# Performance work log

Hardware: AMD Instinct MI355X
Metric: run time of the kernel (lower is better)

## Reference

```python
import jax, jax.numpy as jnp
import numpy as np

N = 10000      # nodes
E = 160000     # edges (before self loops)
F_IN = 78      # atom features
C = 128        # output_dim per head
H = 10         # heads in gat1
G = 64         # graphs in batch


def gat_conv(x, src, dst, n_nodes, W, a_src, a_dst, heads, ch):
    # x: [N, Fin]; W: [Fin, heads*ch]; a_src/a_dst: [heads, ch]
    h = (x @ W).reshape(-1, heads, ch)                      # [N, H, C]
    alpha_src = (h * a_src).sum(-1)                         # [N, H]
    alpha_dst = (h * a_dst).sum(-1)                         # [N, H]
    e = jax.nn.leaky_relu(alpha_src[src] + alpha_dst[dst], 0.2)  # [E, H]
    # segment softmax over edges grouped by destination node
    m = jax.ops.segment_max(e, dst, num_segments=n_nodes)
    m = jnp.where(jnp.isfinite(m), m, 0.0)
    ex = jnp.exp(e - m[dst])
    den = jax.ops.segment_sum(ex, dst, num_segments=n_nodes)
    alpha = ex / (den[dst] + 1e-16)                         # [E, H]
    out = jax.ops.segment_sum(h[src] * alpha[:, :, None], dst,
                              num_segments=n_nodes)          # [N, H, C]
    return out, alpha


def setup_inputs() -> dict:
    key = jax.random.key(0)
    ks = jax.random.split(key, 12)
    x = jax.random.normal(ks[0], (N, F_IN), dtype=jnp.float32)
    edge_index = jax.random.randint(ks[1], (2, E), 0, N, dtype=jnp.int64)
    batch = jnp.sort(jax.random.randint(ks[2], (N,), 0, G, dtype=jnp.int64))
    s1 = 1.0 / np.sqrt(F_IN)
    s2 = 1.0 / np.sqrt(H * C)
    W1 = jax.random.normal(ks[3], (F_IN, H * C), jnp.float32) * s1
    att_src1 = jax.random.normal(ks[4], (H, C), jnp.float32) * 0.1
    att_dst1 = jax.random.normal(ks[5], (H, C), jnp.float32) * 0.1
    b1 = jnp.zeros((H * C,), jnp.float32)
    W2 = jax.random.normal(ks[6], (H * C, C), jnp.float32) * s2
    att_src2 = jax.random.normal(ks[7], (1, C), jnp.float32) * 0.1
    att_dst2 = jax.random.normal(ks[8], (1, C), jnp.float32) * 0.1
    b2 = jnp.zeros((C,), jnp.float32)
    return {"x": x, "edge_index": edge_index, "batch": batch,
            "W1": W1, "att_src1": att_src1, "att_dst1": att_dst1, "b1": b1,
            "W2": W2, "att_src2": att_src2, "att_dst2": att_dst2, "b2": b2}


def reference(x, edge_index, batch, W1, att_src1, att_dst1, b1,
              W2, att_src2, att_dst2, b2):
    n = x.shape[0]
    loops = jnp.arange(n, dtype=edge_index.dtype)
    src = jnp.concatenate([edge_index[0], loops])  # PyG adds self loops
    dst = jnp.concatenate([edge_index[1], loops])
    # layer 1: 10 heads, concat
    h1, alpha1 = gat_conv(x, src, dst, n, W1, att_src1, att_dst1, H, C)
    h1 = jax.nn.elu(h1.reshape(n, H * C) + b1)     # dropout skipped (eval)
    # layer 2: 1 head
    h2, _ = gat_conv(h1, src, dst, n, W2, att_src2, att_dst2, 1, C)
    h2 = jax.nn.elu(h2.reshape(n, C) + b2)
    # global max pool per graph
    pooled = jax.ops.segment_max(h2, batch, num_segments=G)  # [G, C]
    return pooled, alpha1
```

## Files before the change

kernel.cpp:

```cpp
#include <hip/hip_runtime.h>
#include <hip/hip_bf16.h>

#define FIN 78
#define CDIM 128
#define HEADS 10
#define HC 1280
#define GRAPHS 64
#define KP 96

typedef __bf16 bf16x8 __attribute__((ext_vector_type(8)));
typedef __bf16 bf16x4 __attribute__((ext_vector_type(4)));
typedef float f32x4 __attribute__((ext_vector_type(4)));

__global__ void init_kernel(unsigned* counts, unsigned* cursor, unsigned* pooled_u,
                            float* h2p, float* as1, float* ad1, float* as2, float* ad2,
                            const float* __restrict__ x, __bf16* __restrict__ xb,
                            const float* __restrict__ W1, __bf16* __restrict__ W1t,
                            const float* __restrict__ W2, __bf16* __restrict__ W2t,
                            int N, int Mpad) {
    int t = blockIdx.x * 256 + threadIdx.x;
    if (t < N) { counts[t] = 0u; cursor[t] = 0u; as2[t] = 0.f; ad2[t] = 0.f; }
    if (t < GRAPHS * CDIM) pooled_u[t] = 0x007FFFFFu;
    if (t < N * CDIM) h2p[t] = 0.f;
    if (t < N * HEADS) { as1[t] = 0.f; ad1[t] = 0.f; }
    if (t < Mpad * KP) {
        int m = t / KP, k = t % KP;
        float v = (m < N && k < FIN) ? x[(size_t)m * FIN + k] : 0.f;
        xb[t] = (__bf16)v;
    }
    if (t < HC * KP) {
        int n = t / KP, k = t % KP;
        float v = (k < FIN) ? W1[(size_t)k * HC + n] : 0.f;
        W1t[t] = (__bf16)v;
    }
    if (t < CDIM * HC) {
        int n = t / HC, k = t % HC;
        W2t[t] = (__bf16)W2[(size_t)k * CDIM + n];
    }
}

__global__ __launch_bounds__(256) void gemm1_mfma_kernel(
        const __bf16* __restrict__ xb, const __bf16* __restrict__ W1t,
        const float* __restrict__ asrc, const float* __restrict__ adst,
        __bf16* __restrict__ h1pb, float* __restrict__ as1, float* __restrict__ ad1,
        int M) {
    __shared__ __align__(16) __bf16 Alds[128][104];
    __shared__ __align__(16) __bf16 Blds[128][104];
    const int tid = threadIdx.x;
    const int wave = tid >> 6, lane = tid & 63;
    const int wr = wave >> 1, wc = wave & 1;
    const int m0 = blockIdx.x * 128;
    const int head = blockIdx.y;
    const int n0 = head * CDIM;
    const int fl = lane & 15;
    const int fh = lane >> 4;

    for (int idx = tid; idx < 128 * 12; idx += 256) {
        int r = idx / 12, ks = (idx % 12) * 8;
        *(bf16x8*)&Alds[r][ks] = *(const bf16x8*)(xb + (size_t)(m0 + r) * KP + ks);
        *(bf16x8*)&Blds[r][ks] = *(const bf16x8*)(W1t + (size_t)(n0 + r) * KP + ks);
    }
    __syncthreads();

    f32x4 acc[4][4] = {};
    #pragma unroll
    for (int ks = 0; ks < KP; ks += 32) {
        bf16x8 a[4], b[4];
        #pragma unroll
        for (int t = 0; t < 4; ++t) {
            a[t] = *(const bf16x8*)&Alds[wr * 64 + t * 16 + fl][ks + fh * 8];
            b[t] = *(const bf16x8*)&Blds[wc * 64 + t * 16 + fl][ks + fh * 8];
        }
        #pragma unroll
        for (int i = 0; i < 4; ++i)
            #pragma unroll
            for (int j = 0; j < 4; ++j)
                acc[i][j] = __builtin_amdgcn_mfma_f32_16x16x32_bf16(a[i], b[j], acc[i][j], 0, 0, 0);
    }

    float a_s[4], a_d[4];
    #pragma unroll
    for (int j = 0; j < 4; ++j) {
        int gn = n0 + wc * 64 + j * 16 + fl;
        a_s[j] = asrc[gn];
        a_d[j] = adst[gn];
    }
    #pragma unroll
    for (int i = 0; i < 4; ++i) {
        #pragma unroll
        for (int r = 0; r < 4; ++r) {
            int gm = m0 + wr * 64 + i * 16 + fh * 4 + r;
            bool ok = gm < M;
            float vs = 0.f, vd = 0.f;
            #pragma unroll
            for (int j = 0; j < 4; ++j) {
                float v = acc[i][j][r];
                if (ok) h1pb[(size_t)gm * HC + n0 + wc * 64 + j * 16 + fl] = (__bf16)v;
                vs += v * a_s[j];
                vd += v * a_d[j];
            }
            #pragma unroll
            for (int off = 1; off < 16; off <<= 1) {
                vs += __shfl_xor(vs, off);
                vd += __shfl_xor(vd, off);
            }
            if (fl == 0 && ok) {
                atomicAdd(&as1[gm * HEADS + head], vs);
                atomicAdd(&ad1[gm * HEADS + head], vd);
            }
        }
    }
}

__global__ __launch_bounds__(256) void gemm2_mfma_kernel(
        const __bf16* __restrict__ A, const __bf16* __restrict__ W2t,
        const float* __restrict__ asrc2, const float* __restrict__ adst2,
        float* __restrict__ C, float* __restrict__ as2, float* __restrict__ ad2, int M) {
    constexpr int BK = 64;
    constexpr int KCHUNK = HC / 2;
    __shared__ __align__(16) __bf16 Alds[64][BK + 8];
    __shared__ __align__(16) __bf16 Blds[64][BK + 8];
    const int tid = threadIdx.x;
    const int wave = tid >> 6, lane = tid & 63;
    const int wr = wave >> 1, wc = wave & 1;
    const int m0 = blockIdx.x * 64;
    const int n0 = blockIdx.y * 64;
    const int kbase = blockIdx.z * KCHUNK;

    const int kslot = (tid & 7) * 8;
    const int srow  = tid >> 3;
    const int fl = lane & 15;
    const int fh = lane >> 4;

    f32x4 acc[2][2] = {};

    for (int k0 = kbase; k0 < kbase + KCHUNK; k0 += BK) {
        #pragma unroll
        for (int rp = 0; rp < 2; ++rp) {
            int r = srow + rp * 32;
            int gm = m0 + r;
            bf16x8 va = {};
            if (gm < M) va = *(const bf16x8*)(A + (size_t)gm * HC + k0 + kslot);
            *(bf16x8*)&Alds[r][kslot] = va;
            *(bf16x8*)&Blds[r][kslot] = *(const bf16x8*)(W2t + (size_t)(n0 + r) * HC + k0 + kslot);
        }
        __syncthreads();
        #pragma unroll
        for (int ks = 0; ks < BK; ks += 32) {
            bf16x8 a[2], b[2];
            #pragma unroll
            for (int t = 0; t < 2; ++t) {
                a[t] = *(const bf16x8*)&Alds[wr * 32 + t * 16 + fl][ks + fh * 8];
                b[t] = *(const bf16x8*)&Blds[wc * 32 + t * 16 + fl][ks + fh * 8];
            }
            #pragma unroll
            for (int i = 0; i < 2; ++i)
                #pragma unroll
                for (int j = 0; j < 2; ++j)
                    acc[i][j] = __builtin_amdgcn_mfma_f32_16x16x32_bf16(a[i], b[j], acc[i][j], 0, 0, 0);
        }
        __syncthreads();
    }
    const int gn0 = n0 + wc * 32 + fl;
    const int gn1 = gn0 + 16;
    const float a_s0 = asrc2[gn0], a_s1 = asrc2[gn1];
    const float a_d0 = adst2[gn0], a_d1 = adst2[gn1];
    #pragma unroll
    for (int i = 0; i < 2; ++i)
        #pragma unroll
        for (int r = 0; r < 4; ++r) {
            int gm = m0 + wr * 32 + i * 16 + fh * 4 + r;
            if (gm < M) {
                atomicAdd(&C[(size_t)gm * CDIM + gn0], acc[i][0][r]);
                atomicAdd(&C[(size_t)gm * CDIM + gn1], acc[i][1][r]);
            }
            float vs = acc[i][0][r] * a_s0 + acc[i][1][r] * a_s1;
            float vd = acc[i][0][r] * a_d0 + acc[i][1][r] * a_d1;
            #pragma unroll
            for (int off = 1; off < 16; off <<= 1) {
                vs += __shfl_xor(vs, off);
                vd += __shfl_xor(vd, off);
            }
            if (fl == 0 && gm < M) {
                atomicAdd(&as2[gm], vs);
                atomicAdd(&ad2[gm], vd);
            }
        }
}

__global__ void hist_kernel(const int* __restrict__ ei, int E, int N, unsigned* counts) {
    int e = blockIdx.x * 256 + threadIdx.x;
    int Et = E + N;
    if (e >= Et) return;
    int d = (e < E) ? ei[E + e] : (e - E);
    atomicAdd(&counts[d], 1u);
}

__global__ void scan_kernel(const unsigned* __restrict__ counts, unsigned* __restrict__ offsets, int n) {
    __shared__ unsigned part[1024];
    int t = threadIdx.x;
    int chunk = (n + 1023) / 1024;
    int lo = t * chunk, hi = min(lo + chunk, n);
    unsigned s = 0;
    for (int i = lo; i < hi; ++i) s += counts[i];
    part[t] = s;
    __syncthreads();
    for (int d = 1; d < 1024; d <<= 1) {
        unsigned v = (t >= d) ? part[t - d] : 0u;
        __syncthreads();
        part[t] += v;
        __syncthreads();
    }
    unsigned base = (t == 0) ? 0u : part[t - 1];
    for (int i = lo; i < hi; ++i) { offsets[i] = base; base += counts[i]; }
    if (t == 1023) offsets[n] = part[1023];
}

__global__ void scatter_kernel(const int* __restrict__ ei, int E, int N,
                               const unsigned* __restrict__ offsets, unsigned* cursor,
                               int* __restrict__ csr_src, int* __restrict__ csr_eid) {
    int e = blockIdx.x * 256 + threadIdx.x;
    int Et = E + N;
    if (e >= Et) return;
    int s, d;
    if (e < E) { s = ei[e]; d = ei[E + e]; } else { s = e - E; d = e - E; }
    unsigned pos = offsets[d] + atomicAdd(&cursor[d], 1u);
    csr_src[pos] = s;
    csr_eid[pos] = e;
}

__global__ __launch_bounds__(256) void softmax1_kernel(
        const unsigned* __restrict__ offsets,
        const int* __restrict__ csr_src, const int* __restrict__ csr_eid,
        const float* __restrict__ as1, const float* __restrict__ ad1,
        float* __restrict__ alpha_out, float* __restrict__ alpha_csr, int N) {
    const int wave = threadIdx.x >> 6, lane = threadIdx.x & 63;
    const int n = blockIdx.x * 4 + wave;
    if (n >= N) return;
    const unsigned p0 = offsets[n], p1 = offsets[n + 1];
    const unsigned deg = p1 - p0;

    float adn[HEADS];
    #pragma unroll
    for (int h = 0; h < HEADS; ++h) adn[h] = ad1[n * HEADS + h];

    if (deg <= 64) {
        const bool act = lane < (int)deg;
        const unsigned p = p0 + lane;
        int s = 0, eid = 0;
        if (act) { s = csr_src[p]; eid = csr_eid[p]; }
        const float* arow = as1 + (size_t)s * HEADS;
        float e[HEADS];
        #pragma unroll
        for (int h = 0; h < HEADS; ++h) {
            float v = act ? (arow[h] + adn[h]) : -INFINITY;
            e[h] = (v >= 0.f) ? v : 0.2f * v;
        }
        float m[HEADS];
        #pragma unroll
        for (int h = 0; h < HEADS; ++h) m[h] = e[h];
        #pragma unroll
        for (int off = 32; off; off >>= 1)
            #pragma unroll
            for (int h = 0; h < HEADS; ++h) m[h] = fmaxf(m[h], __shfl_xor(m[h], off));
        float ex[HEADS], sm[HEADS];
        #pragma unroll
        for (int h = 0; h < HEADS; ++h) {
            ex[h] = act ? __expf(e[h] - m[h]) : 0.f;
            sm[h] = ex[h];
        }
        #pragma unroll
        for (int off = 32; off; off >>= 1)
            #pragma unroll
            for (int h = 0; h < HEADS; ++h) sm[h] += __shfl_xor(sm[h], off);
        if (act) {
            #pragma unroll
            for (int h = 0; h < HEADS; ++h) {
                float a = ex[h] / (sm[h] + 1e-16f);
                alpha_csr[(size_t)p * HEADS + h] = a;
                alpha_out[(size_t)eid * HEADS + h] = a;
            }
        }
    } else {
        float m[HEADS];
        #pragma unroll
        for (int h = 0; h < HEADS; ++h) m[h] = -INFINITY;
        for (unsigned p = p0 + lane; p < p1; p += 64) {
            const float* arow = as1 + (size_t)csr_src[p] * HEADS;
            #pragma unroll
            for (int h = 0; h < HEADS; ++h) {
                float v = arow[h] + adn[h];
                v = (v >= 0.f) ? v : 0.2f * v;
                m[h] = fmaxf(m[h], v);
            }
        }
        #pragma unroll
        for (int off = 32; off; off >>= 1)
            #pragma unroll
            for (int h = 0; h < HEADS; ++h) m[h] = fmaxf(m[h], __shfl_xor(m[h], off));
        float sm[HEADS];
        #pragma unroll
        for (int h = 0; h < HEADS; ++h) sm[h] = 0.f;
        for (unsigned p = p0 + lane; p < p1; p += 64) {
            const float* arow = as1 + (size_t)csr_src[p] * HEADS;
            #pragma unroll
            for (int h = 0; h < HEADS; ++h) {
                float v = arow[h] + adn[h];
                v = (v >= 0.f) ? v : 0.2f * v;
                sm[h] += __expf(v - m[h]);
            }
        }
        #pragma unroll
        for (int off = 32; off; off >>= 1)
            #pragma unroll
            for (int h = 0; h < HEADS; ++h) sm[h] += __shfl_xor(sm[h], off);
        float inv[HEADS];
        #pragma unroll
        for (int h = 0; h < HEADS; ++h) inv[h] = 1.f / (sm[h] + 1e-16f);
        for (unsigned p = p0 + lane; p < p1; p += 64) {
            const float* arow = as1 + (size_t)csr_src[p] * HEADS;
            int eid = csr_eid[p];
            #pragma unroll
            for (int h = 0; h < HEADS; ++h) {
                float v = arow[h] + adn[h];
                v = (v >= 0.f) ? v : 0.2f * v;
                float a = __expf(v - m[h]) * inv[h];
                alpha_csr[(size_t)p * HEADS + h] = a;
                alpha_out[(size_t)eid * HEADS + h] = a;
            }
        }
    }
}

__global__ __launch_bounds__(320) void agg1_kernel(
        const unsigned* __restrict__ offsets, const int* __restrict__ csr_src,
        const float* __restrict__ alpha_csr, const __bf16* __restrict__ h1pb,
        const float* __restrict__ b1, __bf16* __restrict__ h1b, int N) {
    __shared__ float a_lds[64 * HEADS];
    __shared__ int s_lds[64];
    int n = blockIdx.x;
    unsigned p0 = offsets[n], p1 = offsets[n + 1];
    int tid = threadIdx.x;
    const int col = tid * 4;
    const int hd = tid >> 5;
    float acc[4] = {0.f, 0.f, 0.f, 0.f};
    for (unsigned base = p0; base < p1; base += 64) {
        int cnt = (int)min(64u, p1 - base);
        for (int idx = tid; idx < cnt * HEADS; idx += 320)
            a_lds[idx] = alpha_csr[(size_t)base * HEADS + idx];
        for (int idx = tid; idx < cnt; idx += 320) s_lds[idx] = csr_src[base + idx];
        __syncthreads();
        for (int j = 0; j < cnt; ++j) {
            bf16x4 hv = *(const bf16x4*)(h1pb + (size_t)s_lds[j] * HC + col);
            float a = a_lds[j * HEADS + hd];
            #pragma unroll
            for (int k = 0; k < 4; ++k) acc[k] += (float)hv[k] * a;
        }
        __syncthreads();
    }
    const float4 bv = *(const float4*)(b1 + col);
    bf16x4 outv;
    float vb[4] = {bv.x, bv.y, bv.z, bv.w};
    #pragma unroll
    for (int k = 0; k < 4; ++k) {
        float v = acc[k] + vb[k];
        v = (v > 0.f) ? v : expm1f(v);
        outv[k] = (__bf16)v;
    }
    *(bf16x4*)(h1b + (size_t)n * HC + col) = outv;
}

__device__ __forceinline__ unsigned enc_f(float f) {
    unsigned b = __float_as_uint(f);
    return (b & 0x80000000u) ? ~b : (b | 0x80000000u);
}
__device__ __forceinline__ float dec_f(unsigned k) {
    return (k & 0x80000000u) ? __uint_as_float(k & 0x7FFFFFFFu) : __uint_as_float(~k);
}

__global__ __launch_bounds__(128) void agg2_kernel(
        const unsigned* __restrict__ offsets, const int* __restrict__ csr_src,
        const float* __restrict__ as2, const float* __restrict__ ad2,
        const float* __restrict__ h2p, const float* __restrict__ b2,
        const int* __restrict__ batch, unsigned* __restrict__ pooled_u, int N) {
    const int n = blockIdx.x;
    const int tid = threadIdx.x;
    const int lane = tid & 63;
    const unsigned p0 = offsets[n], p1 = offsets[n + 1];
    const int deg = (int)(p1 - p0);
    const float adn = ad2[n];
    float acc = 0.f;

    if (deg <= 64) {
        int s_reg = 0;
        float e_reg = -INFINITY;
        if (lane < deg) {
            s_reg = csr_src[p0 + lane];
            float v = as2[s_reg] + adn;
            e_reg = (v >= 0.f) ? v : 0.2f * v;
        }
        float m = e_reg;
        #pragma unroll
        for (int off = 32; off; off >>= 1) m = fmaxf(m, __shfl_xor(m, off));
        float ex = (lane < deg) ? __expf(e_reg - m) : 0.f;
        float den = ex;
        #pragma unroll
        for (int off = 32; off; off >>= 1) den += __shfl_xor(den, off);
        float inv = 1.f / (den + 1e-16f);
        for (int j = 0; j < deg; ++j) {
            int sj = __shfl(s_reg, j);
            float aj = __shfl(ex, j) * inv;
            acc += h2p[(size_t)sj * CDIM + tid] * aj;
        }
    } else {
        float m = -INFINITY;
        for (unsigned p = p0 + lane; p < p1; p += 64) {
            float v = as2[csr_src[p]] + adn;
            v = (v >= 0.f) ? v : 0.2f * v;
            m = fmaxf(m, v);
        }
        #pragma unroll
        for (int off = 32; off; off >>= 1) m = fmaxf(m, __shfl_xor(m, off));
        float den = 0.f;
        for (unsigned p = p0 + lane; p < p1; p += 64) {
            float v = as2[csr_src[p]] + adn;
            v = (v >= 0.f) ? v : 0.2f * v;
            den += __expf(v - m);
        }
        #pragma unroll
        for (int off = 32; off; off >>= 1) den += __shfl_xor(den, off);
        float inv = 1.f / (den + 1e-16f);
        for (unsigned p = p0; p < p1; ++p) {
            int sj = csr_src[p];
            float v = as2[sj] + adn;
            v = (v >= 0.f) ? v : 0.2f * v;
            float aj = __expf(v - m) * inv;
            acc += h2p[(size_t)sj * CDIM + tid] * aj;
        }
    }
    float v = acc + b2[tid];
    v = (v > 0.f) ? v : expm1f(v);
    atomicMax(&pooled_u[batch[n] * CDIM + tid], enc_f(v));
}

__global__ void pool_write_kernel(const unsigned* __restrict__ pooled_u, float* __restrict__ out) {
    int t = blockIdx.x * 256 + threadIdx.x;
    if (t < GRAPHS * CDIM) out[t] = dec_f(pooled_u[t]);
}

extern "C" void kernel_launch(void* const* d_in, const int* in_sizes, int n_in,
                              void* d_out, int out_size, void* d_ws, size_t ws_size,
                              hipStream_t stream) {
    const float* x     = (const float*)d_in[0];
    const int*   ei    = (const int*)d_in[1];
    const int*   batch = (const int*)d_in[2];
    const float* W1    = (const float*)d_in[3];
    const float* asrc1 = (const float*)d_in[4];
    const float* adst1 = (const float*)d_in[5];
    const float* b1    = (const float*)d_in[6];
    const float* W2    = (const float*)d_in[7];
    const float* asrc2 = (const float*)d_in[8];
    const float* adst2 = (const float*)d_in[9];
    const float* b2    = (const float*)d_in[10];
    float* out = (float*)d_out;

    const int N  = in_sizes[0] / FIN;
    const int E  = in_sizes[1] / 2;
    const int Et = E + N;
    const int Mpad = ((N + 127) / 128) * 128;

    char* w = (char*)d_ws;
    auto alloc = [&](size_t nbytes) {
        char* p = w;
        w += (nbytes + 255) & ~(size_t)255;
        return p;
    };
    __bf16* h1pb = (__bf16*)alloc((size_t)N * HC * 2);
    __bf16* h1b  = (__bf16*)alloc((size_t)N * HC * 2);
    __bf16* xb   = (__bf16*)alloc((size_t)Mpad * KP * 2);
    __bf16* W1t  = (__bf16*)alloc((size_t)HC * KP * 2);
    __bf16* W2t  = (__bf16*)alloc((size_t)CDIM * HC * 2);
    float*  h2p  = (float*)alloc((size_t)N * CDIM * 4);
    float*  as1  = (float*)alloc((size_t)N * HEADS * 4);
    float*  ad1  = (float*)alloc((size_t)N * HEADS * 4);
    float*  as2  = (float*)alloc((size_t)N * 4);
    float*  ad2  = (float*)alloc((size_t)N * 4);
    float*  alpha_csr = (float*)alloc((size_t)Et * HEADS * 4);
    unsigned* counts  = (unsigned*)alloc((size_t)N * 4);
    unsigned* cursor  = (unsigned*)alloc((size_t)N * 4);
    unsigned* offsets = (unsigned*)alloc((size_t)(N + 1) * 4);
    int* csr_src = (int*)alloc((size_t)Et * 4);
    int* csr_eid = (int*)alloc((size_t)Et * 4);
    unsigned* pooled_u = (unsigned*)alloc((size_t)GRAPHS * CDIM * 4);

    float* alpha_out = out + GRAPHS * CDIM;

    init_kernel<<<(N * CDIM + 255) / 256, 256, 0, stream>>>(
        counts, cursor, pooled_u, h2p, as1, ad1, as2, ad2,
        x, xb, W1, W1t, W2, W2t, N, Mpad);

    gemm1_mfma_kernel<<<dim3(Mpad / 128, HEADS), 256, 0, stream>>>(
        xb, W1t, asrc1, adst1, h1pb, as1, ad1, N);

    hist_kernel<<<(Et + 255) / 256, 256, 0, stream>>>(ei, E, N, counts);
    scan_kernel<<<1, 1024, 0, stream>>>(counts, offsets, N);
    scatter_kernel<<<(Et + 255) / 256, 256, 0, stream>>>(ei, E, N, offsets, cursor, csr_src, csr_eid);

    softmax1_kernel<<<(N + 3) / 4, 256, 0, stream>>>(
        offsets, csr_src, csr_eid, as1, ad1, alpha_out, alpha_csr, N);
    agg1_kernel<<<N, 320, 0, stream>>>(offsets, csr_src, alpha_csr, h1pb, b1, h1b, N);

    gemm2_mfma_kernel<<<dim3((N + 63) / 64, CDIM / 64, 2), 256, 0, stream>>>(
        h1b, W2t, asrc2, adst2, h2p, as2, ad2, N);

    agg2_kernel<<<N, 128, 0, stream>>>(offsets, csr_src, as2, ad2, h2p, b2, batch, pooled_u, N);

    pool_write_kernel<<<(GRAPHS * CDIM + 255) / 256, 256, 0, stream>>>(pooled_u, out);
}
```

Baseline: 277.9 us.

## Stage GEMM epilogues through LDS, replace split-K atomics with partials plus combine

```diff
diff --git a/kernel.cpp b/kernel.cpp
--- a/kernel.cpp
+++ b/kernel.cpp
@@ -13,15 +13,14 @@
 typedef float f32x4 __attribute__((ext_vector_type(4)));
 
 __global__ void init_kernel(unsigned* counts, unsigned* cursor, unsigned* pooled_u,
-                            float* h2p, float* as1, float* ad1, float* as2, float* ad2,
+                            float* as1, float* ad1,
                             const float* __restrict__ x, __bf16* __restrict__ xb,
                             const float* __restrict__ W1, __bf16* __restrict__ W1t,
                             const float* __restrict__ W2, __bf16* __restrict__ W2t,
                             int N, int Mpad) {
     int t = blockIdx.x * 256 + threadIdx.x;
-    if (t < N) { counts[t] = 0u; cursor[t] = 0u; as2[t] = 0.f; ad2[t] = 0.f; }
+    if (t < N) { counts[t] = 0u; cursor[t] = 0u; }
     if (t < GRAPHS * CDIM) pooled_u[t] = 0x007FFFFFu;
-    if (t < N * CDIM) h2p[t] = 0.f;
     if (t < N * HEADS) { as1[t] = 0.f; ad1[t] = 0.f; }
     if (t < Mpad * KP) {
         int m = t / KP, k = t % KP;
@@ -44,8 +43,9 @@
         const float* __restrict__ asrc, const float* __restrict__ adst,
         __bf16* __restrict__ h1pb, float* __restrict__ as1, float* __restrict__ ad1,
         int M) {
-    __shared__ __align__(16) __bf16 Alds[128][104];
-    __shared__ __align__(16) __bf16 Blds[128][104];
+    __shared__ __align__(16) __bf16 smem[2 * 128 * 104];
+    auto Alds = (__bf16 (*)[104])smem;
+    auto Blds = (__bf16 (*)[104])(smem + 128 * 104);
     const int tid = threadIdx.x;
     const int wave = tid >> 6, lane = tid & 63;
     const int wr = wave >> 1, wc = wave & 1;
@@ -90,36 +90,50 @@
         #pragma unroll
         for (int r = 0; r < 4; ++r) {
             int gm = m0 + wr * 64 + i * 16 + fh * 4 + r;
-            bool ok = gm < M;
             float vs = 0.f, vd = 0.f;
             #pragma unroll
             for (int j = 0; j < 4; ++j) {
-                float v = acc[i][j][r];
-                if (ok) h1pb[(size_t)gm * HC + n0 + wc * 64 + j * 16 + fl] = (__bf16)v;
-                vs += v * a_s[j];
-                vd += v * a_d[j];
+                vs += acc[i][j][r] * a_s[j];
+                vd += acc[i][j][r] * a_d[j];
             }
             #pragma unroll
             for (int off = 1; off < 16; off <<= 1) {
                 vs += __shfl_xor(vs, off);
                 vd += __shfl_xor(vd, off);
             }
-            if (fl == 0 && ok) {
+            if (fl == 0 && gm < M) {
                 atomicAdd(&as1[gm * HEADS + head], vs);
                 atomicAdd(&ad1[gm * HEADS + head], vd);
             }
         }
     }
+
+    __syncthreads();
+    auto Cst = (__bf16 (*)[136])smem;
+    #pragma unroll
+    for (int i = 0; i < 4; ++i)
+        #pragma unroll
+        for (int j = 0; j < 4; ++j)
+            #pragma unroll
+            for (int r = 0; r < 4; ++r)
+                Cst[wr * 64 + i * 16 + fh * 4 + r][wc * 64 + j * 16 + fl] = (__bf16)acc[i][j][r];
+    __syncthreads();
+    for (int idx = tid; idx < 128 * 16; idx += 256) {
+        int r = idx >> 4, v = (idx & 15) * 8;
+        int gm = m0 + r;
+        if (gm < M)
+            *(bf16x8*)(h1pb + (size_t)gm * HC + n0 + v) = *(const bf16x8*)&Cst[r][v];
+    }
 }
 
 __global__ __launch_bounds__(256) void gemm2_mfma_kernel(
         const __bf16* __restrict__ A, const __bf16* __restrict__ W2t,
-        const float* __restrict__ asrc2, const float* __restrict__ adst2,
-        float* __restrict__ C, float* __restrict__ as2, float* __restrict__ ad2, int M) {
+        float* __restrict__ Cpart, int M) {
     constexpr int BK = 64;
     constexpr int KCHUNK = HC / 2;
-    __shared__ __align__(16) __bf16 Alds[64][BK + 8];
-    __shared__ __align__(16) __bf16 Blds[64][BK + 8];
+    __shared__ __align__(16) __bf16 smem[2 * 64 * 72];
+    auto Alds = (__bf16 (*)[72])smem;
+    auto Blds = (__bf16 (*)[72])(smem + 64 * 72);
     const int tid = threadIdx.x;
     const int wave = tid >> 6, lane = tid & 63;
     const int wr = wave >> 1, wc = wave & 1;
@@ -161,31 +175,45 @@
         }
         __syncthreads();
     }
-    const int gn0 = n0 + wc * 32 + fl;
-    const int gn1 = gn0 + 16;
-    const float a_s0 = asrc2[gn0], a_s1 = asrc2[gn1];
-    const float a_d0 = adst2[gn0], a_d1 = adst2[gn1];
+    auto CstF = (float (*)[68])smem;
     #pragma unroll
     for (int i = 0; i < 2; ++i)
         #pragma unroll
-        for (int r = 0; r < 4; ++r) {
-            int gm = m0 + wr * 32 + i * 16 + fh * 4 + r;
-            if (gm < M) {
-                atomicAdd(&C[(size_t)gm * CDIM + gn0], acc[i][0][r]);
-                atomicAdd(&C[(size_t)gm * CDIM + gn1], acc[i][1][r]);
-            }
-            float vs = acc[i][0][r] * a_s0 + acc[i][1][r] * a_s1;
-            float vd = acc[i][0][r] * a_d0 + acc[i][1][r] * a_d1;
-            #pragma unroll
-            for (int off = 1; off < 16; off <<= 1) {
-                vs += __shfl_xor(vs, off);
-                vd += __shfl_xor(vd, off);
-            }
-            if (fl == 0 && gm < M) {
-                atomicAdd(&as2[gm], vs);
-                atomicAdd(&ad2[gm], vd);
-            }
-        }
+        for (int j = 0; j < 2; ++j)
+            #pragma unroll
+            for (int r = 0; r < 4; ++r)
+                CstF[wr * 32 + i * 16 + fh * 4 + r][wc * 32 + j * 16 + fl] = acc[i][j][r];
+    __syncthreads();
+    float* base = Cpart + (size_t)blockIdx.z * M * CDIM;
+    for (int idx = tid; idx < 64 * 16; idx += 256) {
+        int r = idx >> 4, c = (idx & 15) * 4;
+        int gm = m0 + r;
+        if (gm < M)
+            *(f32x4*)(base + (size_t)gm * CDIM + n0 + c) = *(const f32x4*)&CstF[r][c];
+    }
+}
+
+__global__ __launch_bounds__(256) void combine_kernel(
+        const float* __restrict__ Cpart, const float* __restrict__ asrc2,
+        const float* __restrict__ adst2, __bf16* __restrict__ h2b,
+        float* __restrict__ as2, float* __restrict__ ad2, int N) {
+    const int lane = threadIdx.x & 63, wave = threadIdx.x >> 6;
+    const int n = blockIdx.x * 4 + wave;
+    if (n >= N) return;
+    const float* p0 = Cpart + (size_t)n * CDIM;
+    const float* p1 = Cpart + (size_t)(N + n) * CDIM;
+    float v0 = p0[lane] + p1[lane];
+    float v1 = p0[lane + 64] + p1[lane + 64];
+    h2b[(size_t)n * CDIM + lane] = (__bf16)v0;
+    h2b[(size_t)n * CDIM + lane + 64] = (__bf16)v1;
+    float vs = v0 * asrc2[lane] + v1 * asrc2[lane + 64];
+    float vd = v0 * adst2[lane] + v1 * adst2[lane + 64];
+    #pragma unroll
+    for (int off = 32; off; off >>= 1) {
+        vs += __shfl_xor(vs, off);
+        vd += __shfl_xor(vd, off);
+    }
+    if (lane == 0) { as2[n] = vs; ad2[n] = vd; }
 }
 
 __global__ void hist_kernel(const int* __restrict__ ei, int E, int N, unsigned* counts) {
@@ -381,7 +409,7 @@
 __global__ __launch_bounds__(128) void agg2_kernel(
         const unsigned* __restrict__ offsets, const int* __restrict__ csr_src,
         const float* __restrict__ as2, const float* __restrict__ ad2,
-        const float* __restrict__ h2p, const float* __restrict__ b2,
+        const __bf16* __restrict__ h2b, const float* __restrict__ b2,
         const int* __restrict__ batch, unsigned* __restrict__ pooled_u, int N) {
     const int n = blockIdx.x;
     const int tid = threadIdx.x;
@@ -410,7 +438,7 @@
         for (int j = 0; j < deg; ++j) {
             int sj = __shfl(s_reg, j);
             float aj = __shfl(ex, j) * inv;
-            acc += h2p[(size_t)sj * CDIM + tid] * aj;
+            acc += (float)h2b[(size_t)sj * CDIM + tid] * aj;
         }
     } else {
         float m = -INFINITY;
@@ -435,7 +463,7 @@
             float v = as2[sj] + adn;
             v = (v >= 0.f) ? v : 0.2f * v;
             float aj = __expf(v - m) * inv;
-            acc += h2p[(size_t)sj * CDIM + tid] * aj;
+            acc += (float)h2b[(size_t)sj * CDIM + tid] * aj;
         }
     }
     float v = acc + b2[tid];
@@ -480,7 +508,8 @@
     __bf16* xb   = (__bf16*)alloc((size_t)Mpad * KP * 2);
     __bf16* W1t  = (__bf16*)alloc((size_t)HC * KP * 2);
     __bf16* W2t  = (__bf16*)alloc((size_t)CDIM * HC * 2);
-    float*  h2p  = (float*)alloc((size_t)N * CDIM * 4);
+    float*  Cpart = (float*)alloc((size_t)2 * N * CDIM * 4);
+    __bf16* h2b  = (__bf16*)alloc((size_t)N * CDIM * 2);
     float*  as1  = (float*)alloc((size_t)N * HEADS * 4);
     float*  ad1  = (float*)alloc((size_t)N * HEADS * 4);
     float*  as2  = (float*)alloc((size_t)N * 4);
@@ -495,9 +524,9 @@
 
     float* alpha_out = out + GRAPHS * CDIM;
 
-    init_kernel<<<(N * CDIM + 255) / 256, 256, 0, stream>>>(
-        counts, cursor, pooled_u, h2p, as1, ad1, as2, ad2,
-        x, xb, W1, W1t, W2, W2t, N, Mpad);
+    const int init_work = Mpad * KP;
+    init_kernel<<<(init_work + 255) / 256, 256, 0, stream>>>(
+        counts, cursor, pooled_u, as1, ad1, x, xb, W1, W1t, W2, W2t, N, Mpad);
 
     gemm1_mfma_kernel<<<dim3(Mpad / 128, HEADS), 256, 0, stream>>>(
         xb, W1t, asrc1, adst1, h1pb, as1, ad1, N);
@@ -511,9 +540,10 @@
     agg1_kernel<<<N, 320, 0, stream>>>(offsets, csr_src, alpha_csr, h1pb, b1, h1b, N);
 
     gemm2_mfma_kernel<<<dim3((N + 63) / 64, CDIM / 64, 2), 256, 0, stream>>>(
-        h1b, W2t, asrc2, adst2, h2p, as2, ad2, N);
-
-    agg2_kernel<<<N, 128, 0, stream>>>(offsets, csr_src, as2, ad2, h2p, b2, batch, pooled_u, N);
+        h1b, W2t, Cpart, N);
+    combine_kernel<<<(N + 3) / 4, 256, 0, stream>>>(Cpart, asrc2, adst2, h2b, as2, ad2, N);
+
+    agg2_kernel<<<N, 128, 0, stream>>>(offsets, csr_src, as2, ad2, h2b, b2, batch, pooled_u, N);
 
     pool_write_kernel<<<(GRAPHS * CDIM + 255) / 256, 256, 0, stream>>>(pooled_u, out);
 }
```

After: 273.2 us. Within noise of the previous version (-1.7%).
